# Optimization experiments

Measured on AMD Instinct MI355X. Metric: run time of the kernel, lower is better.

Reference implementation:

```python
import jax, jax.numpy as jnp
import numpy as np

B, T, D, H, F = 4, 2048, 1024, 16, 4096
HD = D // H
EPS = 1e-5


def setup_inputs() -> dict:
    key = jax.random.key(0)
    ks = jax.random.split(key, 10)
    s = lambda fan_in: 1.0 / np.sqrt(fan_in)
    return {
        "x": jax.random.normal(ks[0], (B, T, D), jnp.float32),
        "ln1_g": jnp.ones((D,), jnp.float32),
        "ln1_b": jnp.zeros((D,), jnp.float32),
        "ln2_g": jnp.ones((D,), jnp.float32),
        "ln2_b": jnp.zeros((D,), jnp.float32),
        "Wq": jax.random.normal(ks[1], (H, D, HD), jnp.float32) * s(D),
        "Wk": jax.random.normal(ks[2], (H, D, HD), jnp.float32) * s(D),
        "Wv": jax.random.normal(ks[3], (H, D, HD), jnp.float32) * s(D),
        "Wo": jax.random.normal(ks[4], (D, D), jnp.float32) * s(D),
        "bo": jnp.zeros((D,), jnp.float32),
        "W1": jax.random.normal(ks[5], (D, F), jnp.float32) * s(D),
        "b1": jnp.zeros((F,), jnp.float32),
        "W2": jax.random.normal(ks[6], (F, D), jnp.float32) * s(F),
        "b2": jnp.zeros((D,), jnp.float32),
    }


def _layernorm(x, g, b):
    mu = jnp.mean(x, axis=-1, keepdims=True)
    var = jnp.mean(jnp.square(x - mu), axis=-1, keepdims=True)
    return (x - mu) * jax.lax.rsqrt(var + EPS) * g + b


def reference(x, ln1_g, ln1_b, ln2_g, ln2_b, Wq, Wk, Wv, Wo, bo, W1, b1, W2, b2):
    Bc, Tc, Dc = x.shape
    xn = _layernorm(x, ln1_g, ln1_b)
    # per-head projections (source loops over heads; here batched over h)
    q = jnp.einsum('btd,hdk->bhtk', xn, Wq)
    k = jnp.einsum('btd,hdk->bhtk', xn, Wk)
    v = jnp.einsum('btd,hdk->bhtk', xn, Wv)
    scale = jnp.asarray(Dc, x.dtype) ** -0.5  # C**-0.5 with C = embedding_dim
    scores = jnp.einsum('bhtk,bhsk->bhts', q, k) * scale
    causal = jnp.tril(jnp.ones((Tc, Tc), bool))
    scores = jnp.where(causal, scores, -jnp.inf)
    attn = jax.nn.softmax(scores, axis=-1)
    out = jnp.einsum('bhts,bhsk->bhtk', attn, v)
    out = out.transpose(0, 2, 1, 3).reshape(Bc, Tc, Dc)  # concat heads
    attn_out = out @ Wo + bo
    h = attn_out + x  # residual 1
    hn = _layernorm(h, ln2_g, ln2_b)
    ff = jax.nn.relu(hn @ W1 + b1) @ W2 + b2
    return ff + h  # residual 2
```

## Files before the change

kernel.cpp:

```cpp
#include <hip/hip_runtime.h>
#include <hip/hip_bf16.h>

#define NB 4
#define NT 2048
#define ND 1024
#define NH 16
#define NHD 64
#define NF 4096
#define MTOK (NB*NT)

typedef float f32x4 __attribute__((ext_vector_type(4)));
typedef __bf16 bf16x8 __attribute__((ext_vector_type(8)));
typedef short s16x8 __attribute__((ext_vector_type(8)));
typedef unsigned short ushort_t;

__device__ inline ushort_t f2bf(float f) {
    unsigned int u = __builtin_bit_cast(unsigned int, f);
    unsigned int r = (u + 0x7FFFu + ((u >> 16) & 1u)) >> 16;
    return (ushort_t)r;
}
__device__ inline float bf2f(ushort_t u) {
    return __builtin_bit_cast(float, (unsigned int)u << 16);
}

__device__ __forceinline__ void async_load16(const void* g, void* l) {
    __builtin_amdgcn_global_load_lds(
        (const __attribute__((address_space(1))) void*)g,
        (__attribute__((address_space(3))) void*)l, 16, 0, 0);
}

__device__ __forceinline__ unsigned int cvt_pk_bf16(float lo, float hi) {
    unsigned int r;
    asm("v_cvt_pk_bf16_f32 %0, %1, %2" : "=v"(r) : "v"(lo), "v"(hi));
    return r;
}

__device__ __forceinline__ float exp2_fast(float x) {
    float r;
    asm("v_exp_f32 %0, %1" : "=v"(r) : "v"(x));
    return r;
}

__global__ __launch_bounds__(256)
void transpose_to_bf16(const float* __restrict__ src, ushort_t* __restrict__ dst,
                       int R, int C) {
    __shared__ float tile[32][33];
    int c0 = blockIdx.x * 32, r0 = blockIdx.y * 32;
    #pragma unroll
    for (int i = 0; i < 32; i += 8)
        tile[threadIdx.y + i][threadIdx.x] =
            src[(size_t)(r0 + threadIdx.y + i) * C + c0 + threadIdx.x];
    __syncthreads();
    #pragma unroll
    for (int i = 0; i < 32; i += 8)
        dst[(size_t)(c0 + threadIdx.y + i) * R + r0 + threadIdx.x] =
            f2bf(tile[threadIdx.x][threadIdx.y + i]);
}

__global__ __launch_bounds__(256)
void transpose_qkv_to_bf16(const float* __restrict__ Wq, const float* __restrict__ Wk,
                           const float* __restrict__ Wv, ushort_t* __restrict__ dst) {
    __shared__ float tile[32][33];
    int z = blockIdx.z;
    int w = z >> 4, h = z & 15;
    const float* src = (w == 0 ? Wq : (w == 1 ? Wk : Wv)) + (size_t)h * ND * NHD;
    const float sc = (w == 0) ? 0.03125f * 1.44269504f : 1.0f;
    ushort_t* out = dst + ((size_t)w * ND + h * NHD) * ND;
    int c0 = blockIdx.x * 32, r0 = blockIdx.y * 32;
    #pragma unroll
    for (int i = 0; i < 32; i += 8)
        tile[threadIdx.y + i][threadIdx.x] =
            src[(size_t)(r0 + threadIdx.y + i) * NHD + c0 + threadIdx.x];
    __syncthreads();
    #pragma unroll
    for (int i = 0; i < 32; i += 8)
        out[(size_t)(c0 + threadIdx.y + i) * ND + r0 + threadIdx.x] =
            f2bf(tile[threadIdx.x][threadIdx.y + i] * sc);
}

__global__ __launch_bounds__(256)
void layernorm_to_bf16(const float* __restrict__ x, const float* __restrict__ g,
                       const float* __restrict__ bvec, ushort_t* __restrict__ out) {
    int row = blockIdx.x;
    const float4* xr = (const float4*)(x + (size_t)row * ND);
    float4 v = xr[threadIdx.x];
    float s = v.x + v.y + v.z + v.w;
    float s2 = v.x * v.x + v.y * v.y + v.z * v.z + v.w * v.w;
    #pragma unroll
    for (int o = 32; o >= 1; o >>= 1) {
        s += __shfl_xor(s, o);
        s2 += __shfl_xor(s2, o);
    }
    __shared__ float red[8];
    int wave = threadIdx.x >> 6, lane = threadIdx.x & 63;
    if (lane == 0) { red[wave] = s; red[4 + wave] = s2; }
    __syncthreads();
    float ts = red[0] + red[1] + red[2] + red[3];
    float ts2 = red[4] + red[5] + red[6] + red[7];
    float mu = ts * (1.f / ND);
    float var = ts2 * (1.f / ND) - mu * mu;
    float rs = rsqrtf(var + 1e-5f);
    float4 gv = ((const float4*)g)[threadIdx.x];
    float4 bv = ((const float4*)bvec)[threadIdx.x];
    ushort4 o4;
    o4.x = f2bf((v.x - mu) * rs * gv.x + bv.x);
    o4.y = f2bf((v.y - mu) * rs * gv.y + bv.y);
    o4.z = f2bf((v.z - mu) * rs * gv.z + bv.z);
    o4.w = f2bf((v.w - mu) * rs * gv.w + bv.w);
    ((ushort4*)(out + (size_t)row * ND))[threadIdx.x] = o4;
}

__global__ __launch_bounds__(256)
void layernorm_bf16(const ushort_t* __restrict__ x, const float* __restrict__ g,
                    const float* __restrict__ bvec, ushort_t* __restrict__ out) {
    int row = blockIdx.x;
    ushort4 u4 = ((const ushort4*)(x + (size_t)row * ND))[threadIdx.x];
    float4 v;
    v.x = bf2f(u4.x); v.y = bf2f(u4.y); v.z = bf2f(u4.z); v.w = bf2f(u4.w);
    float s = v.x + v.y + v.z + v.w;
    float s2 = v.x * v.x + v.y * v.y + v.z * v.z + v.w * v.w;
    #pragma unroll
    for (int o = 32; o >= 1; o >>= 1) {
        s += __shfl_xor(s, o);
        s2 += __shfl_xor(s2, o);
    }
    __shared__ float red[8];
    int wave = threadIdx.x >> 6, lane = threadIdx.x & 63;
    if (lane == 0) { red[wave] = s; red[4 + wave] = s2; }
    __syncthreads();
    float ts = red[0] + red[1] + red[2] + red[3];
    float ts2 = red[4] + red[5] + red[6] + red[7];
    float mu = ts * (1.f / ND);
    float var = ts2 * (1.f / ND) - mu * mu;
    float rs = rsqrtf(var + 1e-5f);
    float4 gv = ((const float4*)g)[threadIdx.x];
    float4 bv = ((const float4*)bvec)[threadIdx.x];
    ushort4 o4;
    o4.x = f2bf((v.x - mu) * rs * gv.x + bv.x);
    o4.y = f2bf((v.y - mu) * rs * gv.y + bv.y);
    o4.z = f2bf((v.z - mu) * rs * gv.z + bv.z);
    o4.w = f2bf((v.w - mu) * rs * gv.w + bv.w);
    ((ushort4*)(out + (size_t)row * ND))[threadIdx.x] = o4;
}

template<bool HAS_BIAS, bool RELU, int RES_MODE, bool OUT_F32>
__global__ __launch_bounds__(512, 2)
void gemm8p(const ushort_t* __restrict__ A, const ushort_t* __restrict__ Bt,
            const float* __restrict__ bias, const void* __restrict__ res,
            void* __restrict__ outp, int M, int N, int K) {
    constexpr int BN = 256;
    constexpr int NFR = BN / 64;
    __shared__ __align__(16) ushort_t As[2][256 * 64];
    __shared__ __align__(16) ushort_t Bs[2][BN * 64];
    const int t = threadIdx.x;
    const int wave = t >> 6, lane = t & 63;
    const int wm = wave >> 2, wn = wave & 3;
    const int g = lane >> 4, l16 = lane & 15;
    int wid = blockIdx.y * gridDim.x + blockIdx.x;
    const int cpx = (gridDim.x * gridDim.y) >> 3;
    wid = (wid & 7) * cpx + (wid >> 3);
    const int m0 = (wid / gridDim.x) * 256;
    const int n0 = (wid % gridDim.x) * BN;
    const int lrow8 = lane >> 3;
    const int srcCol = ((lane & 7) ^ lrow8) * 8;
    const ushort_t* Abase = A + (size_t)m0 * K + srcCol;
    const ushort_t* Bbase = Bt + (size_t)n0 * K + srcCol;
    const int NKT = K >> 6;

    f32x4 acc[8][NFR] = {};

    auto stageAhalf = [&](int kt, int h, int slot) {
        #pragma unroll
        for (int j = 2 * h; j < 2 * h + 2; j++) {
            const int rowbase = j * 64 + wave * 8;
            async_load16(Abase + (size_t)(rowbase + lrow8) * K + kt * 64,
                         &As[slot][rowbase * 64]);
        }
    };
    auto stageBhalf = [&](int kt, int h, int slot) {
        #pragma unroll
        for (int j = 2 * h; j < 2 * h + 2; j++) {
            const int rowbase = j * 64 + wave * 8;
            async_load16(Bbase + (size_t)(rowbase + lrow8) * K + kt * 64,
                         &Bs[slot][rowbase * 64]);
        }
    };

    stageAhalf(0, 0, 0); stageAhalf(0, 1, 0);
    stageBhalf(0, 0, 0); stageBhalf(0, 1, 0);
    stageBhalf(1, 0, 1); stageBhalf(1, 1, 1);
    stageAhalf(1, 0, 1);
    asm volatile("s_waitcnt vmcnt(6)" ::: "memory");
    __builtin_amdgcn_s_barrier();
    __builtin_amdgcn_sched_barrier(0);

    for (int kt = 0; kt < NKT; ++kt) {
        const int cur = kt & 1, nxt = cur ^ 1;
        const ushort_t* as = As[cur];
        const ushort_t* bs = Bs[cur];
        bf16x8 bfr[NFR][2];
        #pragma unroll
        for (int q = 0; q < 4; q++) {
            if (q == 0) {
                #pragma unroll
                for (int nf = 0; nf < NFR; nf++)
                    #pragma unroll
                    for (int ks = 0; ks < 2; ks++) {
                        const int row = wn * (BN / 4) + nf * 16 + l16;
                        int a = row * 128 + ks * 64 + 16 * g;
                        a ^= (row & 7) << 4;
                        bfr[nf][ks] = *(const bf16x8*)((const char*)bs + a);
                    }
            }
            bf16x8 af[2][2];
            #pragma unroll
            for (int mi2 = 0; mi2 < 2; mi2++)
                #pragma unroll
                for (int ks = 0; ks < 2; ks++) {
                    const int row = q * 64 + wm * 32 + mi2 * 16 + l16;
                    int a = row * 128 + ks * 64 + 16 * g;
                    a ^= (row & 7) << 4;
                    af[mi2][ks] = *(const bf16x8*)((const char*)as + a);
                }
            if (q == 0)      { if (kt + 1 < NKT) stageAhalf(kt + 1, 1, nxt); }
            else if (q == 1) { if (kt + 2 < NKT) stageBhalf(kt + 2, 0, cur); }
            else if (q == 2) { if (kt + 2 < NKT) stageBhalf(kt + 2, 1, cur); }
            else             { if (kt + 2 < NKT) stageAhalf(kt + 2, 0, cur); }
            __builtin_amdgcn_sched_barrier(0);
            if (q == 3) {
                if (kt >= NKT - 2) asm volatile("s_waitcnt vmcnt(0)" ::: "memory");
                else               asm volatile("s_waitcnt vmcnt(6)" ::: "memory");
            }
            __builtin_amdgcn_s_barrier();
            __builtin_amdgcn_sched_barrier(0);
            __builtin_amdgcn_s_setprio(1);
            #pragma unroll
            for (int mi2 = 0; mi2 < 2; mi2++)
                #pragma unroll
                for (int nf = 0; nf < NFR; nf++)
                    #pragma unroll
                    for (int ks = 0; ks < 2; ks++)
                        acc[q * 2 + mi2][nf] = __builtin_amdgcn_mfma_f32_16x16x32_bf16(
                            af[mi2][ks], bfr[nf][ks], acc[q * 2 + mi2][nf], 0, 0, 0);
            __builtin_amdgcn_s_setprio(0);
            __builtin_amdgcn_s_barrier();
            __builtin_amdgcn_sched_barrier(0);
        }
    }

    const int gc0 = n0 + wn * (BN / 4) + l16;
    #pragma unroll
    for (int mi = 0; mi < 8; mi++) {
        const int rowb = m0 + (mi >> 1) * 64 + wm * 32 + (mi & 1) * 16 + g * 4;
        #pragma unroll
        for (int nf = 0; nf < NFR; nf++) {
            const int col = gc0 + nf * 16;
            float bb = 0.f;
            if constexpr (HAS_BIAS) bb = bias[col];
            #pragma unroll
            for (int r = 0; r < 4; r++) {
                const int row = rowb + r;
                float v = acc[mi][nf][r] + bb;
                if constexpr (RELU) v = fmaxf(v, 0.f);
                if constexpr (RES_MODE == 1)
                    v += ((const float*)res)[(size_t)row * N + col];
                else if constexpr (RES_MODE == 2)
                    v += bf2f(((const ushort_t*)res)[(size_t)row * N + col]);
                if constexpr (OUT_F32)
                    ((float*)outp)[(size_t)row * N + col] = v;
                else
                    ((ushort_t*)outp)[(size_t)row * N + col] = f2bf(v);
            }
        }
    }
}

template<bool HAS_BIAS, bool RELU, int RES_MODE, bool OUT_F32>
__global__ __launch_bounds__(512, 2)
void gemm128(const ushort_t* __restrict__ A, const ushort_t* __restrict__ Bt,
             const float* __restrict__ bias, const void* __restrict__ res,
             void* __restrict__ outp, int M, int N, int K) {
    __shared__ __align__(16) ushort_t As[2][128 * 64];
    __shared__ __align__(16) ushort_t Bs[2][256 * 64];
    const int t = threadIdx.x;
    const int wave = t >> 6, lane = t & 63;
    const int wm = wave >> 2, wn = wave & 3;
    const int g = lane >> 4, l16 = lane & 15;
    int wid = blockIdx.y * gridDim.x + blockIdx.x;
    const int cpx = (gridDim.x * gridDim.y) >> 3;
    wid = (wid & 7) * cpx + (wid >> 3);
    const int m0 = (wid / gridDim.x) * 128;
    const int n0 = (wid % gridDim.x) * 256;
    const int lrow8 = lane >> 3;
    const int srcCol = ((lane & 7) ^ lrow8) * 8;
    const ushort_t* Abase = A + (size_t)m0 * K + srcCol;
    const ushort_t* Bbase = Bt + (size_t)n0 * K + srcCol;
    const int NKT = K >> 6;

    f32x4 acc[4][4] = {};

    auto stageAhalf = [&](int kt, int h, int slot) {
        const int rowbase = h * 64 + wave * 8;
        async_load16(Abase + (size_t)(rowbase + lrow8) * K + kt * 64,
                     &As[slot][rowbase * 64]);
    };
    auto stageBhalf = [&](int kt, int h, int slot) {
        #pragma unroll
        for (int j = 2 * h; j < 2 * h + 2; j++) {
            const int rowbase = j * 64 + wave * 8;
            async_load16(Bbase + (size_t)(rowbase + lrow8) * K + kt * 64,
                         &Bs[slot][rowbase * 64]);
        }
    };

    stageAhalf(0, 0, 0); stageAhalf(0, 1, 0);
    stageBhalf(0, 0, 0); stageBhalf(0, 1, 0);
    stageBhalf(1, 0, 1); stageBhalf(1, 1, 1);
    stageAhalf(1, 0, 1);
    asm volatile("s_waitcnt vmcnt(5)" ::: "memory");
    __builtin_amdgcn_s_barrier();
    __builtin_amdgcn_sched_barrier(0);

    for (int kt = 0; kt < NKT; ++kt) {
        const int cur = kt & 1, nxt = cur ^ 1;
        const ushort_t* as = As[cur];
        const ushort_t* bs = Bs[cur];
        bf16x8 bfr[4][2];
        #pragma unroll
        for (int ph = 0; ph < 2; ph++) {
            if (ph == 0) {
                #pragma unroll
                for (int nf = 0; nf < 4; nf++)
                    #pragma unroll
                    for (int ks = 0; ks < 2; ks++) {
                        const int row = wn * 64 + nf * 16 + l16;
                        int a = row * 128 + ks * 64 + 16 * g;
                        a ^= (row & 7) << 4;
                        bfr[nf][ks] = *(const bf16x8*)((const char*)bs + a);
                    }
            }
            bf16x8 af[2][2];
            #pragma unroll
            for (int mi2 = 0; mi2 < 2; mi2++)
                #pragma unroll
                for (int ks = 0; ks < 2; ks++) {
                    const int row = ph * 64 + wm * 32 + mi2 * 16 + l16;
                    int a = row * 128 + ks * 64 + 16 * g;
                    a ^= (row & 7) << 4;
                    af[mi2][ks] = *(const bf16x8*)((const char*)as + a);
                }
            if (ph == 0) {
                if (kt + 1 < NKT) stageAhalf(kt + 1, 1, nxt);
            } else {
                if (kt + 2 < NKT) {
                    stageBhalf(kt + 2, 0, cur);
                    stageBhalf(kt + 2, 1, cur);
                    stageAhalf(kt + 2, 0, cur);
                }
            }
            __builtin_amdgcn_sched_barrier(0);
            if (ph == 1) {
                if (kt >= NKT - 2) asm volatile("s_waitcnt vmcnt(0)" ::: "memory");
                else               asm volatile("s_waitcnt vmcnt(5)" ::: "memory");
            }
            __builtin_amdgcn_s_barrier();
            __builtin_amdgcn_sched_barrier(0);
            __builtin_amdgcn_s_setprio(1);
            #pragma unroll
            for (int mi2 = 0; mi2 < 2; mi2++)
                #pragma unroll
                for (int nf = 0; nf < 4; nf++)
                    #pragma unroll
                    for (int ks = 0; ks < 2; ks++)
                        acc[ph * 2 + mi2][nf] = __builtin_amdgcn_mfma_f32_16x16x32_bf16(
                            af[mi2][ks], bfr[nf][ks], acc[ph * 2 + mi2][nf], 0, 0, 0);
            __builtin_amdgcn_s_setprio(0);
            __builtin_amdgcn_s_barrier();
            __builtin_amdgcn_sched_barrier(0);
        }
    }

    const int gc0 = n0 + wn * 64 + l16;
    #pragma unroll
    for (int mi = 0; mi < 4; mi++) {
        const int rowb = m0 + (mi >> 1) * 64 + wm * 32 + (mi & 1) * 16 + g * 4;
        #pragma unroll
        for (int nf = 0; nf < 4; nf++) {
            const int col = gc0 + nf * 16;
            float bb = 0.f;
            if constexpr (HAS_BIAS) bb = bias[col];
            #pragma unroll
            for (int r = 0; r < 4; r++) {
                const int row = rowb + r;
                float v = acc[mi][nf][r] + bb;
                if constexpr (RELU) v = fmaxf(v, 0.f);
                if constexpr (RES_MODE == 1)
                    v += ((const float*)res)[(size_t)row * N + col];
                else if constexpr (RES_MODE == 2)
                    v += bf2f(((const ushort_t*)res)[(size_t)row * N + col]);
                if constexpr (OUT_F32)
                    ((float*)outp)[(size_t)row * N + col] = v;
                else
                    ((ushort_t*)outp)[(size_t)row * N + col] = f2bf(v);
            }
        }
    }
}

__global__ __launch_bounds__(256)
void attn_kernel(const ushort_t* __restrict__ qkv, ushort_t* __restrict__ out) {
    __shared__ __align__(16) ushort_t Ks[2][64 * 64];
    __shared__ __align__(16) ushort_t Vt[2][64 * 64];
    __shared__ unsigned int Pw[4][32][35];
    const int L = blockIdx.y * gridDim.x + blockIdx.x;
    const int xcd = L & 7, kk = L >> 3;
    const int bh = ((kk & 7) << 3) | xcd;
    const int pairIdx = kk >> 3;
    const int b = bh >> 4, h = bh & 15;
    const int t = threadIdx.x, wave = t >> 6, lane = t & 63;
    const int g = lane >> 4, q16 = lane & 15;
    const size_t base = ((size_t)b * NT) * 3072 + h * NHD;
    const ushort_t* qp_base = qkv + base;
    const ushort_t* kb = qkv + base + 1024;
    const ushort_t* vb = qkv + base + 2048;
    const int krw = lane >> 3, kck = lane & 7;
    const int ksrc = (kck ^ krw) * 8;
    const int vkp = t >> 3, vdg = t & 7;

    bf16x8 ones_f;
    {
        uint4 u = {0x3F803F80u, 0x3F803F80u, 0x3F803F80u, 0x3F803F80u};
        ones_f = __builtin_bit_cast(bf16x8, u);
    }

    auto stageK = [&](int kv, int buf) {
        #pragma unroll
        for (int c = 0; c < 2; c++) {
            const int rowbase = c * 32 + wave * 8;
            async_load16(kb + (size_t)(kv * 64 + rowbase + krw) * 3072 + ksrc,
                         &Ks[buf][rowbase * 64]);
        }
    };
    auto loadV = [&](int kv, s16x8& v0, s16x8& v1) {
        const ushort_t* vp = vb + (size_t)(kv * 64 + 2 * vkp) * 3072 + vdg * 8;
        v0 = *(const s16x8*)vp;
        v1 = *(const s16x8*)(vp + 3072);
    };
    auto writeV = [&](int buf, const s16x8& v0, const s16x8& v1) {
        const uint4 w0 = __builtin_bit_cast(uint4, v0);
        const uint4 w1 = __builtin_bit_cast(uint4, v1);
        const unsigned int lw0[4] = {w0.x, w0.y, w0.z, w0.w};
        const unsigned int lw1[4] = {w1.x, w1.y, w1.z, w1.w};
        #pragma unroll
        for (int j = 0; j < 4; j++) {
            unsigned int we = __builtin_amdgcn_perm(lw1[j], lw0[j], 0x05040100u);
            unsigned int wo = __builtin_amdgcn_perm(lw1[j], lw0[j], 0x07060302u);
            int d0 = vdg * 8 + 2 * j;
            int a0 = (d0 << 7) + (vkp << 2);
            a0 ^= ((((d0) & 7) ^ (((d0) >> 3) & 7)) << 4);
            *(unsigned int*)((char*)&Vt[buf][0] + a0) = we;
            int d1 = d0 + 1;
            int a1 = (d1 << 7) + (vkp << 2);
            a1 ^= ((((d1) & 7) ^ (((d1) >> 3) & 7)) << 4);
            *(unsigned int*)((char*)&Vt[buf][0] + a1) = wo;
        }
    };

    for (int half = 0; half < 2; half++) {
        const int qt = half ? (15 - pairIdx) : pairIdx;
        const int q0 = qt * 128;
        const int wq0 = q0 + wave * 32;
        bf16x8 qf[2][2];
        #pragma unroll
        for (int qb2 = 0; qb2 < 2; qb2++) {
            const ushort_t* qp = qp_base + (size_t)(wq0 + 16 * qb2 + q16) * 3072 + 8 * g;
            qf[qb2][0] = *(const bf16x8*)qp;
            qf[qb2][1] = *(const bf16x8*)(qp + 32);
        }
        f32x4 of[2][4] = {};
        f32x4 of4[2] = {};
        const int nkv = 2 * qt + 2;

        {
            s16x8 pv0, pv1;
            stageK(0, 0);
            loadV(0, pv0, pv1);
            asm volatile("s_waitcnt vmcnt(0)" ::: "memory");
            writeV(0, pv0, pv1);
        }
        __syncthreads();

        for (int kv = 0; kv < nkv; ++kv) {
            const int cur = kv & 1, nxt = cur ^ 1;
            s16x8 pv0, pv1;
            const bool pre = (kv + 1 < nkv);
            if (pre) {
                stageK(kv + 1, nxt);
                loadV(kv + 1, pv0, pv1);
            }
            __builtin_amdgcn_sched_barrier(0);

            const int kbase = kv * 64;
            if (kbase <= wq0 + 31) {
                bf16x8 kf[4][2];
                #pragma unroll
                for (int n = 0; n < 4; n++)
                    #pragma unroll
                    for (int kd = 0; kd < 2; kd++) {
                        int row = n * 16 + q16;
                        int a = row * 128 + (kd * 64 + 16 * g);
                        a ^= ((row & 7) << 4);
                        kf[n][kd] = *(const bf16x8*)((const char*)&Ks[cur][0] + a);
                    }

                f32x4 sf[2][4] = {};
                #pragma unroll
                for (int n = 0; n < 4; n++)
                    #pragma unroll
                    for (int kd = 0; kd < 2; kd++) {
                        sf[0][n] = __builtin_amdgcn_mfma_f32_16x16x32_bf16(
                            kf[n][kd], qf[0][kd], sf[0][n], 0, 0, 0);
                        sf[1][n] = __builtin_amdgcn_mfma_f32_16x16x32_bf16(
                            kf[n][kd], qf[1][kd], sf[1][n], 0, 0, 0);
                    }

                #pragma unroll
                for (int qb2 = 0; qb2 < 2; qb2++) {
                    const int wqb = wq0 + 16 * qb2 + q16;
                    const bool partial = (kbase + 63 > wq0 + 16 * qb2);
                    float p[4][4];
                    #pragma unroll
                    for (int n = 0; n < 4; n++)
                        #pragma unroll
                        for (int r = 0; r < 4; r++) {
                            float v = sf[qb2][n][r];
                            if (partial) {
                                int kg = kbase + n * 16 + 4 * g + r;
                                if (kg > wqb) v = -1.0e30f;
                            }
                            p[n][r] = exp2_fast(v);
                        }
                    unsigned int* pr = &Pw[wave][16 * qb2 + q16][0];
                    #pragma unroll
                    for (int n = 0; n < 4; n++) {
                        pr[8 * n + 2 * g + 0] = cvt_pk_bf16(p[n][0], p[n][1]);
                        pr[8 * n + 2 * g + 1] = cvt_pk_bf16(p[n][2], p[n][3]);
                    }
                }

                #pragma unroll
                for (int kbk = 0; kbk < 2; kbk++) {
                    bf16x8 pfr[2];
                    #pragma unroll
                    for (int qb2 = 0; qb2 < 2; qb2++) {
                        const unsigned int* pr = &Pw[wave][16 * qb2 + q16][0];
                        uint4 pu;
                        pu.x = pr[16 * kbk + 4 * g + 0];
                        pu.y = pr[16 * kbk + 4 * g + 1];
                        pu.z = pr[16 * kbk + 4 * g + 2];
                        pu.w = pr[16 * kbk + 4 * g + 3];
                        pfr[qb2] = __builtin_bit_cast(bf16x8, pu);
                    }
                    of4[0] = __builtin_amdgcn_mfma_f32_16x16x32_bf16(
                        ones_f, pfr[0], of4[0], 0, 0, 0);
                    of4[1] = __builtin_amdgcn_mfma_f32_16x16x32_bf16(
                        ones_f, pfr[1], of4[1], 0, 0, 0);
                    #pragma unroll
                    for (int nf = 0; nf < 4; nf++) {
                        const int d = nf * 16 + q16;
                        int a = (d << 7) + (kbk * 64 + 16 * g);
                        a ^= (((d & 7) ^ ((d >> 3) & 7)) << 4);
                        bf16x8 vf = *(const bf16x8*)((const char*)&Vt[cur][0] + a);
                        of[0][nf] = __builtin_amdgcn_mfma_f32_16x16x32_bf16(
                            vf, pfr[0], of[0][nf], 0, 0, 0);
                        of[1][nf] = __builtin_amdgcn_mfma_f32_16x16x32_bf16(
                            vf, pfr[1], of[1][nf], 0, 0, 0);
                    }
                }
            }

            if (pre) writeV(nxt, pv0, pv1);
            __syncthreads();
        }

        #pragma unroll
        for (int qb2 = 0; qb2 < 2; qb2++) {
            float rl = 1.f / of4[qb2][0];
            const size_t orow = (size_t)b * NT + q0 + wave * 32 + 16 * qb2 + q16;
            #pragma unroll
            for (int nf = 0; nf < 4; nf++) {
                ushort4 o4;
                o4.x = f2bf(of[qb2][nf][0] * rl);
                o4.y = f2bf(of[qb2][nf][1] * rl);
                o4.z = f2bf(of[qb2][nf][2] * rl);
                o4.w = f2bf(of[qb2][nf][3] * rl);
                *(ushort4*)(out + orow * ND + h * NHD + nf * 16 + 4 * g) = o4;
            }
        }
    }
}

extern "C" void kernel_launch(void* const* d_in, const int* in_sizes, int n_in,
                              void* d_out, int out_size, void* d_ws, size_t ws_size,
                              hipStream_t stream) {
    const float* x     = (const float*)d_in[0];
    const float* ln1_g = (const float*)d_in[1];
    const float* ln1_b = (const float*)d_in[2];
    const float* ln2_g = (const float*)d_in[3];
    const float* ln2_b = (const float*)d_in[4];
    const float* Wq    = (const float*)d_in[5];
    const float* Wk    = (const float*)d_in[6];
    const float* Wv    = (const float*)d_in[7];
    const float* Wo    = (const float*)d_in[8];
    const float* bo    = (const float*)d_in[9];
    const float* W1    = (const float*)d_in[10];
    const float* b1    = (const float*)d_in[11];
    const float* W2    = (const float*)d_in[12];
    const float* b2    = (const float*)d_in[13];
    float* outp = (float*)d_out;

    char* w = (char*)d_ws;
    ushort_t* Wqkv_t = (ushort_t*)(w);
    ushort_t* Wo_t   = (ushort_t*)(w + 6291456);
    ushort_t* W1_t   = (ushort_t*)(w + 8388608);
    ushort_t* W2_t   = (ushort_t*)(w + 16777216);
    ushort_t* xn     = (ushort_t*)(w + 25165824);
    ushort_t* qkv    = (ushort_t*)(w + 41943040);
    ushort_t* attn_o = qkv + (size_t)MTOK * 3072;
    ushort_t* ff1    = qkv;
    ushort_t* hbuf   = (ushort_t*)(w + 41943040 + 67108864);

    dim3 tb(32, 8);
    transpose_qkv_to_bf16<<<dim3(2, 32, 48), tb, 0, stream>>>(Wq, Wk, Wv, Wqkv_t);
    transpose_to_bf16<<<dim3(32, 32), tb, 0, stream>>>(Wo, Wo_t, 1024, 1024);
    transpose_to_bf16<<<dim3(128, 32), tb, 0, stream>>>(W1, W1_t, 1024, 4096);
    transpose_to_bf16<<<dim3(32, 128), tb, 0, stream>>>(W2, W2_t, 4096, 1024);

    layernorm_to_bf16<<<MTOK, 256, 0, stream>>>(x, ln1_g, ln1_b, xn);

    gemm128<false, false, 0, false><<<dim3(12, 64), 512, 0, stream>>>(
        xn, Wqkv_t, nullptr, nullptr, qkv, MTOK, 3072, 1024);

    attn_kernel<<<dim3(8, 64), 256, 0, stream>>>(qkv, attn_o);

    gemm128<true, false, 1, false><<<dim3(4, 64), 512, 0, stream>>>(
        attn_o, Wo_t, bo, x, hbuf, MTOK, 1024, 1024);

    layernorm_bf16<<<MTOK, 256, 0, stream>>>(hbuf, ln2_g, ln2_b, xn);

    gemm8p<true, true, 0, false><<<dim3(16, 32), 512, 0, stream>>>(
        xn, W1_t, b1, nullptr, ff1, MTOK, NF, 1024);

    gemm128<true, false, 2, true><<<dim3(4, 64), 512, 0, stream>>>(
        ff1, W2_t, b2, hbuf, outp, MTOK, 1024, NF);
}
```

Before: 360.2 us.

## Replace 128x256 GEMM with smaller 128x128 tile, K=32 double-buffered kernel

Swaps the 512-thread 128x256 GEMM, which used a two-phase K=64 pipeline, for a 256-thread 128x128 kernel with K=32 tiles and a simple two-slot async prefetch. It is used for the QKV, output-projection and FF2 GEMMs. The aim is more blocks and higher occupancy (launch bounds 256,4) with less LDS per block, so the small-N GEMMs fill the GPU better. In exchange, global-to-LDS traffic goes up because each tile is smaller, each K step has more barriers relative to the MFMA work, and the careful phase-interleaved scheduling is lost.

```diff
diff --git a/kernel.cpp b/kernel.cpp
--- a/kernel.cpp
+++ b/kernel.cpp
@@ -276,114 +276,88 @@
 }
 
 template<bool HAS_BIAS, bool RELU, int RES_MODE, bool OUT_F32>
-__global__ __launch_bounds__(512, 2)
-void gemm128(const ushort_t* __restrict__ A, const ushort_t* __restrict__ Bt,
-             const float* __restrict__ bias, const void* __restrict__ res,
-             void* __restrict__ outp, int M, int N, int K) {
-    __shared__ __align__(16) ushort_t As[2][128 * 64];
-    __shared__ __align__(16) ushort_t Bs[2][256 * 64];
+__global__ __launch_bounds__(256, 4)
+void gemm2b(const ushort_t* __restrict__ A, const ushort_t* __restrict__ Bt,
+            const float* __restrict__ bias, const void* __restrict__ res,
+            void* __restrict__ outp, int M, int N, int K) {
+    __shared__ __align__(16) ushort_t As[2][128 * 32];
+    __shared__ __align__(16) ushort_t Bs[2][128 * 32];
     const int t = threadIdx.x;
     const int wave = t >> 6, lane = t & 63;
-    const int wm = wave >> 2, wn = wave & 3;
+    const int wm = wave >> 1, wn = wave & 1;
     const int g = lane >> 4, l16 = lane & 15;
     int wid = blockIdx.y * gridDim.x + blockIdx.x;
     const int cpx = (gridDim.x * gridDim.y) >> 3;
     wid = (wid & 7) * cpx + (wid >> 3);
     const int m0 = (wid / gridDim.x) * 128;
-    const int n0 = (wid % gridDim.x) * 256;
-    const int lrow8 = lane >> 3;
-    const int srcCol = ((lane & 7) ^ lrow8) * 8;
+    const int n0 = (wid % gridDim.x) * 128;
+    const int rw = lane >> 2, ck = lane & 3;
+    const int srcCol = (ck ^ (rw & 3)) * 8;
     const ushort_t* Abase = A + (size_t)m0 * K + srcCol;
     const ushort_t* Bbase = Bt + (size_t)n0 * K + srcCol;
-    const int NKT = K >> 6;
+    const int NKT = K >> 5;
 
     f32x4 acc[4][4] = {};
 
-    auto stageAhalf = [&](int kt, int h, int slot) {
-        const int rowbase = h * 64 + wave * 8;
-        async_load16(Abase + (size_t)(rowbase + lrow8) * K + kt * 64,
-                     &As[slot][rowbase * 64]);
+    auto stage = [&](int kt, int slot) {
+        #pragma unroll
+        for (int j = 0; j < 2; j++) {
+            const int rowbase = j * 64 + wave * 16;
+            async_load16(Abase + (size_t)(rowbase + rw) * K + kt * 32,
+                         &As[slot][rowbase * 32]);
+        }
+        #pragma unroll
+        for (int j = 0; j < 2; j++) {
+            const int rowbase = j * 64 + wave * 16;
+            async_load16(Bbase + (size_t)(rowbase + rw) * K + kt * 32,
+                         &Bs[slot][rowbase * 32]);
+        }
     };
-    auto stageBhalf = [&](int kt, int h, int slot) {
-        #pragma unroll
-        for (int j = 2 * h; j < 2 * h + 2; j++) {
-            const int rowbase = j * 64 + wave * 8;
-            async_load16(Bbase + (size_t)(rowbase + lrow8) * K + kt * 64,
-                         &Bs[slot][rowbase * 64]);
-        }
-    };
-
-    stageAhalf(0, 0, 0); stageAhalf(0, 1, 0);
-    stageBhalf(0, 0, 0); stageBhalf(0, 1, 0);
-    stageBhalf(1, 0, 1); stageBhalf(1, 1, 1);
-    stageAhalf(1, 0, 1);
-    asm volatile("s_waitcnt vmcnt(5)" ::: "memory");
-    __builtin_amdgcn_s_barrier();
-    __builtin_amdgcn_sched_barrier(0);
+
+    stage(0, 0);
+    stage(1, 1);
 
     for (int kt = 0; kt < NKT; ++kt) {
-        const int cur = kt & 1, nxt = cur ^ 1;
+        const int cur = kt & 1;
+        if (kt >= NKT - 1) asm volatile("s_waitcnt vmcnt(0)" ::: "memory");
+        else               asm volatile("s_waitcnt vmcnt(4)" ::: "memory");
+        __builtin_amdgcn_s_barrier();
+        __builtin_amdgcn_sched_barrier(0);
+
         const ushort_t* as = As[cur];
         const ushort_t* bs = Bs[cur];
-        bf16x8 bfr[4][2];
-        #pragma unroll
-        for (int ph = 0; ph < 2; ph++) {
-            if (ph == 0) {
-                #pragma unroll
-                for (int nf = 0; nf < 4; nf++)
-                    #pragma unroll
-                    for (int ks = 0; ks < 2; ks++) {
-                        const int row = wn * 64 + nf * 16 + l16;
-                        int a = row * 128 + ks * 64 + 16 * g;
-                        a ^= (row & 7) << 4;
-                        bfr[nf][ks] = *(const bf16x8*)((const char*)bs + a);
-                    }
-            }
-            bf16x8 af[2][2];
+        bf16x8 af[4], bfr[4];
+        #pragma unroll
+        for (int mi = 0; mi < 4; mi++) {
+            const int row = wm * 64 + mi * 16 + l16;
+            int a = row * 64 + 16 * g;
+            a ^= (row & 3) << 4;
+            af[mi] = *(const bf16x8*)((const char*)as + a);
+        }
+        #pragma unroll
+        for (int nf = 0; nf < 4; nf++) {
+            const int row = wn * 64 + nf * 16 + l16;
+            int a = row * 64 + 16 * g;
+            a ^= (row & 3) << 4;
+            bfr[nf] = *(const bf16x8*)((const char*)bs + a);
+        }
+        __builtin_amdgcn_s_setprio(1);
+        #pragma unroll
+        for (int mi = 0; mi < 4; mi++)
             #pragma unroll
-            for (int mi2 = 0; mi2 < 2; mi2++)
-                #pragma unroll
-                for (int ks = 0; ks < 2; ks++) {
-                    const int row = ph * 64 + wm * 32 + mi2 * 16 + l16;
-                    int a = row * 128 + ks * 64 + 16 * g;
-                    a ^= (row & 7) << 4;
-                    af[mi2][ks] = *(const bf16x8*)((const char*)as + a);
-                }
-            if (ph == 0) {
-                if (kt + 1 < NKT) stageAhalf(kt + 1, 1, nxt);
-            } else {
-                if (kt + 2 < NKT) {
-                    stageBhalf(kt + 2, 0, cur);
-                    stageBhalf(kt + 2, 1, cur);
-                    stageAhalf(kt + 2, 0, cur);
-                }
-            }
-            __builtin_amdgcn_sched_barrier(0);
-            if (ph == 1) {
-                if (kt >= NKT - 2) asm volatile("s_waitcnt vmcnt(0)" ::: "memory");
-                else               asm volatile("s_waitcnt vmcnt(5)" ::: "memory");
-            }
-            __builtin_amdgcn_s_barrier();
-            __builtin_amdgcn_sched_barrier(0);
-            __builtin_amdgcn_s_setprio(1);
-            #pragma unroll
-            for (int mi2 = 0; mi2 < 2; mi2++)
-                #pragma unroll
-                for (int nf = 0; nf < 4; nf++)
-                    #pragma unroll
-                    for (int ks = 0; ks < 2; ks++)
-                        acc[ph * 2 + mi2][nf] = __builtin_amdgcn_mfma_f32_16x16x32_bf16(
-                            af[mi2][ks], bfr[nf][ks], acc[ph * 2 + mi2][nf], 0, 0, 0);
-            __builtin_amdgcn_s_setprio(0);
-            __builtin_amdgcn_s_barrier();
-            __builtin_amdgcn_sched_barrier(0);
-        }
+            for (int nf = 0; nf < 4; nf++)
+                acc[mi][nf] = __builtin_amdgcn_mfma_f32_16x16x32_bf16(
+                    af[mi], bfr[nf], acc[mi][nf], 0, 0, 0);
+        __builtin_amdgcn_s_setprio(0);
+        __builtin_amdgcn_s_barrier();
+        __builtin_amdgcn_sched_barrier(0);
+        if (kt + 2 < NKT) stage(kt + 2, cur);
     }
 
     const int gc0 = n0 + wn * 64 + l16;
     #pragma unroll
     for (int mi = 0; mi < 4; mi++) {
-        const int rowb = m0 + (mi >> 1) * 64 + wm * 32 + (mi & 1) * 16 + g * 4;
+        const int rowb = m0 + wm * 64 + mi * 16 + g * 4;
         #pragma unroll
         for (int nf = 0; nf < 4; nf++) {
             const int col = gc0 + nf * 16;
@@ -638,12 +612,12 @@
 
     layernorm_to_bf16<<<MTOK, 256, 0, stream>>>(x, ln1_g, ln1_b, xn);
 
-    gemm128<false, false, 0, false><<<dim3(12, 64), 512, 0, stream>>>(
+    gemm2b<false, false, 0, false><<<dim3(24, 64), 256, 0, stream>>>(
         xn, Wqkv_t, nullptr, nullptr, qkv, MTOK, 3072, 1024);
 
     attn_kernel<<<dim3(8, 64), 256, 0, stream>>>(qkv, attn_o);
 
-    gemm128<true, false, 1, false><<<dim3(4, 64), 512, 0, stream>>>(
+    gemm2b<true, false, 1, false><<<dim3(8, 64), 256, 0, stream>>>(
         attn_o, Wo_t, bo, x, hbuf, MTOK, 1024, 1024);
 
     layernorm_bf16<<<MTOK, 256, 0, stream>>>(hbuf, ln2_g, ln2_b, xn);
@@ -651,6 +625,6 @@
     gemm8p<true, true, 0, false><<<dim3(16, 32), 512, 0, stream>>>(
         xn, W1_t, b1, nullptr, ff1, MTOK, NF, 1024);
 
-    gemm128<true, false, 2, true><<<dim3(4, 64), 512, 0, stream>>>(
+    gemm2b<true, false, 2, true><<<dim3(8, 64), 256, 0, stream>>>(
         ff1, W2_t, b2, hbuf, outp, MTOK, 1024, NF);
 }
```

After: 369.1 us. 1.02x slower.
